# Kernel optimization log

Hardware: AMD Instinct MI355X
Metric: run time of the kernel (lower is better)

## Reference

```python
import jax, jax.numpy as jnp
import numpy as np

N, F, T, H, E = 50000, 16, 12, 64, 1600000
OUT = 1


def setup_inputs() -> dict:
    key = jax.random.key(0)
    ks = jax.random.split(key, 14)
    inp = {}
    inp["x"] = jax.random.normal(ks[0], (N, F, T), dtype=jnp.float32)
    inp["edge_index"] = jax.random.randint(ks[1], (2, E), 0, N, dtype=jnp.int32)
    inp["edge_weight"] = jax.random.uniform(ks[2], (E,), dtype=jnp.float32)
    C = F + H  # GCN input channels (x concat hidden)
    s = 0.05
    inp["Wz"] = jax.random.normal(ks[3], (C, H), dtype=jnp.float32) * s
    inp["bz"] = jnp.zeros((H,), dtype=jnp.float32)
    inp["Wr"] = jax.random.normal(ks[4], (C, H), dtype=jnp.float32) * s
    inp["br"] = jnp.zeros((H,), dtype=jnp.float32)
    inp["Wh"] = jax.random.normal(ks[5], (C, H), dtype=jnp.float32) * s
    inp["bh"] = jnp.zeros((H,), dtype=jnp.float32)
    inp["Wa"] = jax.random.normal(ks[6], (H, H), dtype=jnp.float32) * s
    inp["ba"] = jnp.zeros((H,), dtype=jnp.float32)
    inp["cv"] = jax.random.normal(ks[7], (H, 1), dtype=jnp.float32) * s
    inp["Wfc"] = jax.random.normal(ks[8], (H, OUT), dtype=jnp.float32) * s
    inp["bfc"] = jnp.zeros((OUT,), dtype=jnp.float32)
    return inp


def _gcn(xc, W, b, src, dst, ew_norm, self_norm, n):
    # PyG GCNConv: D^{-1/2}(A+I)D^{-1/2} X W + b, with self-loop weight 1
    xw = xc @ W                                   # [N, H]
    msg = xw[src] * ew_norm[:, None]              # [E, H] gather
    agg = jax.ops.segment_sum(msg, dst, num_segments=n)  # scatter-add
    return agg + self_norm[:, None] * xw + b


def reference(x, edge_index, edge_weight, Wz, bz, Wr, br, Wh, bh, Wa, ba, cv, Wfc, bfc):
    n = x.shape[0]
    src, dst = edge_index[0], edge_index[1]
    # symmetric normalization with self-loops (weight 1)
    deg = jax.ops.segment_sum(edge_weight, dst, num_segments=n) + 1.0
    dis = jax.lax.rsqrt(deg)
    ew_norm = dis[src] * edge_weight * dis[dst]
    self_norm = dis * dis

    x_seq = jnp.transpose(x, (2, 0, 1))  # [T, N, F]

    def step(h, x_t):
        xh = jnp.concatenate([x_t, h], axis=1)
        z = jax.nn.sigmoid(_gcn(xh, Wz, bz, src, dst, ew_norm, self_norm, n))
        r = jax.nn.sigmoid(_gcn(xh, Wr, br, src, dst, ew_norm, self_norm, n))
        xrh = jnp.concatenate([x_t, r * h], axis=1)
        hc = jnp.tanh(_gcn(xrh, Wh, bh, src, dst, ew_norm, self_norm, n))
        h_new = z * h + (1.0 - z) * hc
        return h_new, h_new

    h0 = jnp.zeros((n, Wz.shape[1]), dtype=x.dtype)
    _, hs_seq = jax.lax.scan(step, h0, x_seq)      # [T, N, H]

    hs_t = jnp.transpose(hs_seq, (1, 0, 2))        # [N, T, H]
    score = jnp.tanh(hs_t @ Wa + ba)               # [N, T, H]
    align = (score @ cv)[..., 0]                   # [N, T]
    alpha = jax.nn.softmax(align, axis=1)          # softmax over time
    context = jnp.einsum('nt,nth->nh', alpha, hs_t)
    out = context @ Wfc + bfc                      # [N, OUT]
    return out
```

## Files before the change

### kernel.cpp

```cpp
#include <hip/hip_runtime.h>
#include <hip/hip_fp16.h>
#include <math.h>

#define Nn 50000
#define Ff 16
#define Tt 12
#define Hh 64
#define Ee 1600000
#define Cc 80

#define SCAN_NB 98

typedef _Float16 f16x8 __attribute__((ext_vector_type(8)));
typedef float f32x4 __attribute__((ext_vector_type(4)));

static __device__ __forceinline__ float sigmoidf_(float x) { return 1.0f / (1.0f + expf(-x)); }

__global__ void k_deg(const int* __restrict__ ei, const float* __restrict__ ew,
                      unsigned long long* __restrict__ dc) {
  int e = blockIdx.x * blockDim.x + threadIdx.x;
  if (e >= Ee) return;
  int d = ei[Ee + e];
  unsigned long long pk = (1ULL << 42) + (unsigned long long)(ew[e] * 2097152.0f + 0.5f);
  atomicAdd(&dc[d], pk);
}

__global__ void k_dis(const unsigned long long* __restrict__ dc,
                      float* __restrict__ dis, int* __restrict__ cnt) {
  int i = blockIdx.x * blockDim.x + threadIdx.x;
  if (i >= Nn) return;
  unsigned long long v = dc[i];
  cnt[i] = (int)(v >> 42);
  float deg = (float)(v & ((1ULL << 42) - 1)) * (1.0f / 2097152.0f);
  dis[i] = 1.0f / sqrtf(deg + 1.0f);
}

__global__ __launch_bounds__(256) void k_scan1(const int* __restrict__ cnt,
                                               int* __restrict__ bsum) {
  __shared__ int ss[256];
  int b = blockIdx.x, t = threadIdx.x;
  int base = b * 512 + t * 2;
  int s = 0;
  if (base < Nn) s += cnt[base];
  if (base + 1 < Nn) s += cnt[base + 1];
  ss[t] = s;
  __syncthreads();
  for (int off = 128; off > 0; off >>= 1) {
    if (t < off) ss[t] += ss[t + off];
    __syncthreads();
  }
  if (t == 0) bsum[b] = ss[0];
}

__global__ __launch_bounds__(128) void k_scan2(const int* __restrict__ bsum,
                                               int* __restrict__ boff) {
  __shared__ int ss[128];
  int t = threadIdx.x;
  int v = (t < SCAN_NB) ? bsum[t] : 0;
  ss[t] = v;
  __syncthreads();
  for (int off = 1; off < 128; off <<= 1) {
    int u = (t >= off) ? ss[t - off] : 0;
    __syncthreads();
    ss[t] += u;
    __syncthreads();
  }
  if (t < SCAN_NB) boff[t] = ss[t] - v;
}

__global__ __launch_bounds__(256) void k_scan3(const int* __restrict__ cnt,
                                               const int* __restrict__ boff,
                                               int* __restrict__ rp, int* __restrict__ cur) {
  __shared__ int ss[256];
  int b = blockIdx.x, t = threadIdx.x;
  int base = b * 512 + t * 2;
  int c0 = (base < Nn) ? cnt[base] : 0;
  int c1 = (base + 1 < Nn) ? cnt[base + 1] : 0;
  int s = c0 + c1;
  ss[t] = s;
  __syncthreads();
  for (int off = 1; off < 256; off <<= 1) {
    int u = (t >= off) ? ss[t - off] : 0;
    __syncthreads();
    ss[t] += u;
    __syncthreads();
  }
  int run = boff[b] + ss[t] - s;
  if (base < Nn) { rp[base] = run; cur[base] = run; }
  if (base + 1 < Nn) { rp[base + 1] = run + c0; cur[base + 1] = run + c0; }
  if (b == 0 && t == 0) rp[Nn] = Ee;
}

__global__ void k_scatter(const int* __restrict__ ei, const float* __restrict__ ew,
                          const float* __restrict__ dis, int* __restrict__ cur,
                          int2* __restrict__ edge2) {
  int e = blockIdx.x * blockDim.x + threadIdx.x;
  if (e >= Ee) return;
  int s = ei[e];
  int d = ei[Ee + e];
  float w = ew[e] * dis[s] * dis[d];
  int pos = atomicAdd(&cur[d], 1);
  edge2[pos] = make_int2(s, __float_as_int(w));
}

__global__ void k_cvt_x(const float* __restrict__ x, __half* __restrict__ x16) {
  size_t idx = (size_t)blockIdx.x * blockDim.x + threadIdx.x;
  const size_t total = (size_t)Nn * Ff * Tt;
  if (idx < total) x16[idx] = __float2half(x[idx]);
}

__global__ void k_wfrag(const float* __restrict__ Wz, const float* __restrict__ Wr,
                        const float* __restrict__ Wh, __half* __restrict__ frag) {
  int t = blockIdx.x * 256 + threadIdx.x;
  if (t >= 12 * 3 * 64) return;
  int s = t / 192, rem = t % 192, ks = rem / 64, lane = rem % 64;
  int q = lane >> 4, nl = lane & 15;
  const float* W = (s < 4) ? Wz : (s < 8) ? Wr : Wh;
  int n0 = (s & 3) * 16;
  __half tmp[8];
#pragma unroll
  for (int j = 0; j < 8; j++) {
    int k = ks * 32 + q * 8 + j;
    float v = (k < Cc) ? W[k * Hh + n0 + nl] : 0.f;
    tmp[j] = __float2half(v);
  }
  *(uint4*)(frag + ((size_t)(s * 3 + ks) * 64 + lane) * 8) = *(uint4*)tmp;
}

__global__ void k_wfrag_a(const float* __restrict__ Wa, __half* __restrict__ fragA) {
  int t = blockIdx.x * 256 + threadIdx.x;
  if (t >= 8 * 64) return;
  int s = t >> 6, lane = t & 63;
  int tile = s >> 1, ks = s & 1;
  int q = lane >> 4, m = lane & 15;
  __half tmp[8];
#pragma unroll
  for (int j = 0; j < 8; j++) {
    int k = ks * 32 + q * 8 + j;
    tmp[j] = __float2half(Wa[k * Hh + tile * 16 + m]);
  }
  *(uint4*)(fragA + ((size_t)t) * 8) = *(uint4*)tmp;
}

__global__ __launch_bounds__(256) void k_agg_px(
    const float* __restrict__ x, const __half* __restrict__ x16, __half* __restrict__ Px16,
    const int* __restrict__ rp, const int2* __restrict__ edge2,
    const float* __restrict__ dis) {
  int i = blockIdx.x * 4 + (threadIdx.x >> 6);
  if (i >= Nn) return;
  int lane = threadIdx.x & 63;
  const int R = Ff * Tt;
  const bool act = lane < 48;
  float d = dis[i], sn = d * d;
  float a0 = 0.f, a1 = 0.f, a2 = 0.f, a3 = 0.f;
  if (act) {
    float4 sv = *(const float4*)(x + (size_t)i * R + 4 * lane);
    a0 = sn * sv.x; a1 = sn * sv.y; a2 = sn * sv.z; a3 = sn * sv.w;
  }
  int jb = rp[i], je = rp[i + 1];
  for (int j = jb; j < je; j += 2) {
    int jc1 = min(j + 1, Ee - 1);
    int2 e0 = edge2[j];
    int2 e1 = edge2[jc1];
    float w0 = __int_as_float(e0.y);
    float w1 = (j + 1 < je) ? __int_as_float(e1.y) : 0.f;
    if (act) {
      uint2 g0 = *(const uint2*)(x16 + (size_t)e0.x * R + 4 * lane);
      uint2 g1 = *(const uint2*)(x16 + (size_t)e1.x * R + 4 * lane);
      float2 p01 = __half22float2(*reinterpret_cast<const __half2*>(&g0.x));
      float2 p23 = __half22float2(*reinterpret_cast<const __half2*>(&g0.y));
      float2 q01 = __half22float2(*reinterpret_cast<const __half2*>(&g1.x));
      float2 q23 = __half22float2(*reinterpret_cast<const __half2*>(&g1.y));
      a0 = fmaf(w0, p01.x, a0); a1 = fmaf(w0, p01.y, a1);
      a2 = fmaf(w0, p23.x, a2); a3 = fmaf(w0, p23.y, a3);
      a0 = fmaf(w1, q01.x, a0); a1 = fmaf(w1, q01.y, a1);
      a2 = fmaf(w1, q23.x, a2); a3 = fmaf(w1, q23.y, a3);
    }
  }
  if (act) {
#pragma unroll
    for (int k = 0; k < 4; k++) {
      int cch = 4 * lane + k;
      int f = cch / Tt, tt = cch % Tt;
      float val = (k == 0) ? a0 : (k == 1) ? a1 : (k == 2) ? a2 : a3;
      Px16[(size_t)tt * Nn * Ff + (size_t)i * Ff + f] = __float2half(val);
    }
  }
}

__global__ __launch_bounds__(256) void k_agg64v(
    const __half* __restrict__ v, __half* __restrict__ outv,
    const int* __restrict__ rp, const int2* __restrict__ edge2,
    const float* __restrict__ dis) {
  int i = blockIdx.x * 4 + (threadIdx.x >> 6);
  if (i >= Nn) return;
  int lane = threadIdx.x & 63;
  int g = lane >> 4;
  int c = lane & 15;
  float d = dis[i], sn = d * d;
  float a0, a1, a2, a3;
  {
    const uint2 gv = *(const uint2*)(v + (size_t)i * Hh + 4 * c);
    float2 f01 = __half22float2(*reinterpret_cast<const __half2*>(&gv.x));
    float2 f23 = __half22float2(*reinterpret_cast<const __half2*>(&gv.y));
    float ws = (g == 0) ? sn : 0.f;
    a0 = ws * f01.x; a1 = ws * f01.y; a2 = ws * f23.x; a3 = ws * f23.y;
  }
  int jb = rp[i], je = rp[i + 1];
  for (int j0 = jb; j0 < je; j0 += 16) {
    int j1 = j0 + g;
    int j2 = j0 + 4 + g;
    int j3 = j0 + 8 + g;
    int j4 = j0 + 12 + g;
    int2 e1 = edge2[min(j1, Ee - 1)];
    int2 e2 = edge2[min(j2, Ee - 1)];
    int2 e3 = edge2[min(j3, Ee - 1)];
    int2 e4 = edge2[min(j4, Ee - 1)];
    float w1 = (j1 < je) ? __int_as_float(e1.y) : 0.f;
    float w2 = (j2 < je) ? __int_as_float(e2.y) : 0.f;
    float w3 = (j3 < je) ? __int_as_float(e3.y) : 0.f;
    float w4 = (j4 < je) ? __int_as_float(e4.y) : 0.f;
    const uint2 g1 = *(const uint2*)(v + (size_t)e1.x * Hh + 4 * c);
    const uint2 g2 = *(const uint2*)(v + (size_t)e2.x * Hh + 4 * c);
    const uint2 g3 = *(const uint2*)(v + (size_t)e3.x * Hh + 4 * c);
    const uint2 g4 = *(const uint2*)(v + (size_t)e4.x * Hh + 4 * c);
    float2 p01 = __half22float2(*reinterpret_cast<const __half2*>(&g1.x));
    float2 p23 = __half22float2(*reinterpret_cast<const __half2*>(&g1.y));
    float2 q01 = __half22float2(*reinterpret_cast<const __half2*>(&g2.x));
    float2 q23 = __half22float2(*reinterpret_cast<const __half2*>(&g2.y));
    float2 r01 = __half22float2(*reinterpret_cast<const __half2*>(&g3.x));
    float2 r23 = __half22float2(*reinterpret_cast<const __half2*>(&g3.y));
    float2 s01 = __half22float2(*reinterpret_cast<const __half2*>(&g4.x));
    float2 s23 = __half22float2(*reinterpret_cast<const __half2*>(&g4.y));
    a0 = fmaf(w1, p01.x, a0); a1 = fmaf(w1, p01.y, a1);
    a2 = fmaf(w1, p23.x, a2); a3 = fmaf(w1, p23.y, a3);
    a0 = fmaf(w2, q01.x, a0); a1 = fmaf(w2, q01.y, a1);
    a2 = fmaf(w2, q23.x, a2); a3 = fmaf(w2, q23.y, a3);
    a0 = fmaf(w3, r01.x, a0); a1 = fmaf(w3, r01.y, a1);
    a2 = fmaf(w3, r23.x, a2); a3 = fmaf(w3, r23.y, a3);
    a0 = fmaf(w4, s01.x, a0); a1 = fmaf(w4, s01.y, a1);
    a2 = fmaf(w4, s23.x, a2); a3 = fmaf(w4, s23.y, a3);
  }
  a0 += __shfl_xor(a0, 16, 64); a1 += __shfl_xor(a1, 16, 64);
  a2 += __shfl_xor(a2, 16, 64); a3 += __shfl_xor(a3, 16, 64);
  a0 += __shfl_xor(a0, 32, 64); a1 += __shfl_xor(a1, 32, 64);
  a2 += __shfl_xor(a2, 32, 64); a3 += __shfl_xor(a3, 32, 64);
  if (lane < 16) {
    __half2 h01, h23;
    h01.x = __float2half_rn(a0); h01.y = __float2half_rn(a1);
    h23.x = __float2half_rn(a2); h23.y = __float2half_rn(a3);
    uint2 st;
    st.x = *reinterpret_cast<unsigned int*>(&h01);
    st.y = *reinterpret_cast<unsigned int*>(&h23);
    *(uint2*)(outv + (size_t)i * Hh + 4 * c) = st;
  }
}

static __device__ __forceinline__ void stage_x16(
    __half* sX16, const __half* __restrict__ Px16t, const __half* __restrict__ P64,
    int i0, int tid) {
  if (tid < 160) {
    int n = tid / 10, r = tid % 10;
    int i = i0 + n;
    uint4 raw = (r < 2) ? *(const uint4*)(Px16t + (size_t)i * Ff + r * 8)
                        : *(const uint4*)(P64 + (size_t)i * Hh + (r - 2) * 8);
    *(uint4*)(sX16 + n * 104 + r * 8) = raw;
  } else if (tid < 208) {
    int p = tid - 160, n = p / 3, part = p % 3;
    *(uint4*)(sX16 + n * 104 + 80 + part * 8) = make_uint4(0u, 0u, 0u, 0u);
  }
}

__global__ __launch_bounds__(256) void k_gemm_zr(
    const __half* __restrict__ Px16, const __half* __restrict__ Ph16,
    const __half* __restrict__ h16, const __half* __restrict__ frag,
    const float* __restrict__ bz, const float* __restrict__ br,
    __half* __restrict__ zb16, __half* __restrict__ rh16, int tstep) {
  __shared__ __align__(16) __half sX16[16 * 104];
  const int tid = threadIdx.x;
  const int i0 = blockIdx.x * 16;
  const int wv = tid >> 6, lane = tid & 63;
  f16x8 bzf[3], brf[3];
#pragma unroll
  for (int ks = 0; ks < 3; ks++) {
    bzf[ks] = *(const f16x8*)(frag + ((size_t)(wv * 3 + ks) * 64 + lane) * 8);
    brf[ks] = *(const f16x8*)(frag + ((size_t)((4 + wv) * 3 + ks) * 64 + lane) * 8);
  }
  stage_x16(sX16, Px16 + (size_t)tstep * Nn * Ff, Ph16, i0, tid);
  __syncthreads();
  const int m = lane & 15, q = lane >> 4;
  f32x4 accz = {0.f, 0.f, 0.f, 0.f}, accr = {0.f, 0.f, 0.f, 0.f};
#pragma unroll
  for (int ks = 0; ks < 3; ks++) {
    f16x8 a = *(const f16x8*)(sX16 + m * 104 + ks * 32 + q * 8);
    accz = __builtin_amdgcn_mfma_f32_16x16x32_f16(a, bzf[ks], accz, 0, 0, 0);
    accr = __builtin_amdgcn_mfma_f32_16x16x32_f16(a, brf[ks], accr, 0, 0, 0);
  }
  const int o = wv * 16 + m;
  float bzo = bz[o], bro = br[o];
  const int nb = i0 + q * 4;
#pragma unroll
  for (int r = 0; r < 4; r++) {
    int node = nb + r;
    float zv = sigmoidf_(accz[r] + bzo);
    float rv = sigmoidf_(accr[r] + bro);
    float hv = __half2float(h16[(size_t)node * Hh + o]);
    zb16[(size_t)node * Hh + o] = __float2half(zv);
    rh16[(size_t)node * Hh + o] = __float2half(rv * hv);
  }
}

__global__ __launch_bounds__(256) void k_gemm_h(
    const __half* __restrict__ Px16, const __half* __restrict__ Prh16,
    const __half* __restrict__ zb16, float* __restrict__ h, __half* __restrict__ h16,
    __half* __restrict__ hs16, const __half* __restrict__ frag,
    const float* __restrict__ bh, int tstep) {
  __shared__ __align__(16) __half sX16[16 * 104];
  const int tid = threadIdx.x;
  const int i0 = blockIdx.x * 16;
  const int wv = tid >> 6, lane = tid & 63;
  f16x8 bf[3];
#pragma unroll
  for (int ks = 0; ks < 3; ks++)
    bf[ks] = *(const f16x8*)(frag + ((size_t)((8 + wv) * 3 + ks) * 64 + lane) * 8);
  stage_x16(sX16, Px16 + (size_t)tstep * Nn * Ff, Prh16, i0, tid);
  __syncthreads();
  const int m = lane & 15, q = lane >> 4;
  f32x4 acc = {0.f, 0.f, 0.f, 0.f};
#pragma unroll
  for (int ks = 0; ks < 3; ks++) {
    f16x8 a = *(const f16x8*)(sX16 + m * 104 + ks * 32 + q * 8);
    acc = __builtin_amdgcn_mfma_f32_16x16x32_f16(a, bf[ks], acc, 0, 0, 0);
  }
  const int o = wv * 16 + m;
  float bho = bh[o];
  const int nb = i0 + q * 4;
  __half* hst = hs16 + (size_t)tstep * Nn * Hh;
#pragma unroll
  for (int r = 0; r < 4; r++) {
    int node = nb + r;
    float hc = tanhf(acc[r] + bho);
    float zv = __half2float(zb16[(size_t)node * Hh + o]);
    float hv = h[(size_t)node * Hh + o];
    float hn = zv * hv + (1.0f - zv) * hc;
    h[(size_t)node * Hh + o] = hn;
    __half hh = __float2half(hn);
    h16[(size_t)node * Hh + o] = hh;
    hst[(size_t)node * Hh + o] = hh;
  }
}

__global__ __launch_bounds__(256) void k_att(
    const __half* __restrict__ hs16, const __half* __restrict__ fragA,
    const float* __restrict__ ba, const float* __restrict__ cv,
    const float* __restrict__ Wfc, const float* __restrict__ bfc,
    float* __restrict__ out) {
  const int tid = threadIdx.x;
  const int wv = tid >> 6, lane = tid & 63;
  const int i = blockIdx.x * 4 + wv;
  if (i >= Nn) return;
  const int m = lane & 15, q = lane >> 4;

  f16x8 bf[4][2];
#pragma unroll
  for (int s = 0; s < 8; s++)
    bf[s >> 1][s & 1] = *(const f16x8*)(fragA + (size_t)(s * 64 + lane) * 8);

  const int tm = (m < Tt) ? m : (Tt - 1);
  const __half* hbase = hs16 + (size_t)tm * Nn * Hh + (size_t)i * Hh;
  f16x8 a0 = *(const f16x8*)(hbase + q * 8);
  f16x8 a1 = *(const f16x8*)(hbase + 32 + q * 8);

  f32x4 acc[4];
#pragma unroll
  for (int tile = 0; tile < 4; tile++) acc[tile] = f32x4{0.f, 0.f, 0.f, 0.f};
#pragma unroll
  for (int tile = 0; tile < 4; tile++) {
    acc[tile] = __builtin_amdgcn_mfma_f32_16x16x32_f16(a0, bf[tile][0], acc[tile], 0, 0, 0);
    acc[tile] = __builtin_amdgcn_mfma_f32_16x16x32_f16(a1, bf[tile][1], acc[tile], 0, 0, 0);
  }

  float ba_l[4], cv_l[4];
#pragma unroll
  for (int tile = 0; tile < 4; tile++) {
    ba_l[tile] = ba[tile * 16 + m];
    cv_l[tile] = cv[tile * 16 + m];
  }
  float ar[4];
#pragma unroll
  for (int r = 0; r < 4; r++) {
    float s = 0.f;
#pragma unroll
    for (int tile = 0; tile < 4; tile++)
      s += tanhf(acc[tile][r] + ba_l[tile]) * cv_l[tile];
    s += __shfl_xor(s, 1, 64);
    s += __shfl_xor(s, 2, 64);
    s += __shfl_xor(s, 4, 64);
    s += __shfl_xor(s, 8, 64);
    ar[r] = s;
  }
  float al[Tt];
#pragma unroll
  for (int t = 0; t < Tt; t++) al[t] = __shfl(ar[t & 3], (t >> 2) * 16, 64);
  float mx = al[0];
#pragma unroll
  for (int t = 1; t < Tt; t++) mx = fmaxf(mx, al[t]);
  float ssum = 0.f;
#pragma unroll
  for (int t = 0; t < Tt; t++) { al[t] = expf(al[t] - mx); ssum += al[t]; }
  float inv = 1.0f / ssum;
  float cx = 0.f;
#pragma unroll
  for (int t = 0; t < Tt; t++)
    cx = fmaf(al[t], __half2float(hs16[(size_t)t * Nn * Hh + (size_t)i * Hh + lane]), cx);
  float p = cx * inv * Wfc[lane];
#pragma unroll
  for (int off = 32; off >= 1; off >>= 1) p += __shfl_xor(p, off, 64);
  if (lane == 0) out[i] = p + bfc[0];
}

extern "C" void kernel_launch(void* const* d_in, const int* in_sizes, int n_in,
                              void* d_out, int out_size, void* d_ws, size_t ws_size,
                              hipStream_t stream) {
  const float* x   = (const float*)d_in[0];
  const int* ei    = (const int*)d_in[1];
  const float* ew  = (const float*)d_in[2];
  const float* Wz  = (const float*)d_in[3];
  const float* bz  = (const float*)d_in[4];
  const float* Wr  = (const float*)d_in[5];
  const float* br  = (const float*)d_in[6];
  const float* Wh  = (const float*)d_in[7];
  const float* bh  = (const float*)d_in[8];
  const float* Wa  = (const float*)d_in[9];
  const float* ba  = (const float*)d_in[10];
  const float* cv  = (const float*)d_in[11];
  const float* Wfc = (const float*)d_in[12];
  const float* bfc = (const float*)d_in[13];
  float* out = (float*)d_out;

  char* w = (char*)d_ws;
  auto alloc = [&](size_t bytes) {
    char* p = w;
    w += (bytes + 255) & ~(size_t)255;
    return p;
  };
  unsigned long long* dc = (unsigned long long*)alloc((size_t)Nn * 8);
  float* dis = (float*)alloc((size_t)Nn * 4);
  int* cnt   = (int*)alloc((size_t)Nn * 4);
  int* rp    = (int*)alloc((size_t)(Nn + 1) * 4);
  int* cur   = (int*)alloc((size_t)Nn * 4);
  int* bsum  = (int*)alloc((size_t)SCAN_NB * 4);
  int* boff  = (int*)alloc((size_t)SCAN_NB * 4);
  int2* edge2 = (int2*)alloc((size_t)Ee * 8);
  __half* x16  = (__half*)alloc((size_t)Nn * Ff * Tt * 2);
  __half* Px16 = (__half*)alloc((size_t)Tt * Nn * Ff * 2);
  float* h     = (float*)alloc((size_t)Nn * Hh * 4);
  __half* h16  = (__half*)alloc((size_t)Nn * Hh * 2);
  __half* rh16 = (__half*)alloc((size_t)Nn * Hh * 2);
  __half* zb16 = (__half*)alloc((size_t)Nn * Hh * 2);
  __half* Ph16 = (__half*)alloc((size_t)Nn * Hh * 2);
  __half* Prh16 = (__half*)alloc((size_t)Nn * Hh * 2);
  __half* hs16 = (__half*)alloc((size_t)Tt * Nn * Hh * 2);
  __half* wfrag = (__half*)alloc((size_t)12 * 3 * 64 * 8 * 2);
  __half* wfragA = (__half*)alloc((size_t)8 * 64 * 8 * 2);

  hipMemsetAsync(dc, 0, (size_t)Nn * 8, stream);
  hipMemsetAsync(h, 0, (size_t)Nn * Hh * 4, stream);
  hipMemsetAsync(h16, 0, (size_t)Nn * Hh * 2, stream);

  k_deg<<<(Ee + 255) / 256, 256, 0, stream>>>(ei, ew, dc);
  k_dis<<<(Nn + 255) / 256, 256, 0, stream>>>(dc, dis, cnt);
  k_scan1<<<SCAN_NB, 256, 0, stream>>>(cnt, bsum);
  k_scan2<<<1, 128, 0, stream>>>(bsum, boff);
  k_scan3<<<SCAN_NB, 256, 0, stream>>>(cnt, boff, rp, cur);
  k_scatter<<<(Ee + 255) / 256, 256, 0, stream>>>(ei, ew, dis, cur, edge2);
  {
    const size_t total = (size_t)Nn * Ff * Tt;
    k_cvt_x<<<(int)((total + 255) / 256), 256, 0, stream>>>(x, x16);
  }
  k_wfrag<<<9, 256, 0, stream>>>(Wz, Wr, Wh, wfrag);
  k_wfrag_a<<<2, 256, 0, stream>>>(Wa, wfragA);
  k_agg_px<<<(Nn + 3) / 4, 256, 0, stream>>>(x, x16, Px16, rp, edge2, dis);

  const int gGemm = Nn / 16;
  const int gNode = (Nn + 3) / 4;
  for (int t = 0; t < Tt; t++) {
    k_agg64v<<<gNode, 256, 0, stream>>>(h16, Ph16, rp, edge2, dis);
    k_gemm_zr<<<gGemm, 256, 0, stream>>>(Px16, Ph16, h16, wfrag, bz, br, zb16, rh16, t);
    k_agg64v<<<gNode, 256, 0, stream>>>(rh16, Prh16, rp, edge2, dis);
    k_gemm_h<<<gGemm, 256, 0, stream>>>(Px16, Prh16, zb16, h, h16, hs16, wfrag, bh, t);
  }
  k_att<<<gNode, 256, 0, stream>>>(hs16, wfragA, ba, cv, Wfc, bfc, out);
}
```

Baseline: 1.540 ms.

## Fuse neighbor aggregation into GRU gate GEMM kernels via LDS staging

The separate sparse aggregation kernel is folded into the z/r and candidate GEMM kernels. Each wave now aggregates four nodes' neighbor features directly into the shared-memory tile, and that tile feeds the MFMA. This removes the aggregated intermediate buffers, their global write and read-back, and two kernel launches per timestep. The trade-off is coarser parallelism for the gather: each block does sixteen nodes, four per wave serially, so load imbalance and latency hiding may get worse.

```diff
diff --git a/kernel.cpp b/kernel.cpp
--- a/kernel.cpp
+++ b/kernel.cpp
@@ -188,13 +188,22 @@
   }
 }
 
-__global__ __launch_bounds__(256) void k_agg64v(
-    const __half* __restrict__ v, __half* __restrict__ outv,
-    const int* __restrict__ rp, const int2* __restrict__ edge2,
-    const float* __restrict__ dis) {
-  int i = blockIdx.x * 4 + (threadIdx.x >> 6);
-  if (i >= Nn) return;
-  int lane = threadIdx.x & 63;
+static __device__ __forceinline__ void stage_px_zero(
+    __half* sX16, const __half* __restrict__ Px16t, int i0, int tid) {
+  if (tid < 32) {
+    int n = tid >> 1, r = tid & 1;
+    *(uint4*)(sX16 + n * 104 + r * 8) =
+        *(const uint4*)(Px16t + (size_t)(i0 + n) * Ff + r * 8);
+  } else if (tid < 80) {
+    int p = tid - 32, n = p / 3, part = p % 3;
+    *(uint4*)(sX16 + n * 104 + 80 + part * 8) = make_uint4(0u, 0u, 0u, 0u);
+  }
+}
+
+static __device__ __forceinline__ void agg_node_to_lds(
+    __half* sX16, int n, int i, int lane,
+    const __half* __restrict__ v, const int* __restrict__ rp,
+    const int2* __restrict__ edge2, const float* __restrict__ dis) {
   int g = lane >> 4;
   int c = lane & 15;
   float d = dis[i], sn = d * d;
@@ -252,29 +261,16 @@
     uint2 st;
     st.x = *reinterpret_cast<unsigned int*>(&h01);
     st.y = *reinterpret_cast<unsigned int*>(&h23);
-    *(uint2*)(outv + (size_t)i * Hh + 4 * c) = st;
-  }
-}
-
-static __device__ __forceinline__ void stage_x16(
-    __half* sX16, const __half* __restrict__ Px16t, const __half* __restrict__ P64,
-    int i0, int tid) {
-  if (tid < 160) {
-    int n = tid / 10, r = tid % 10;
-    int i = i0 + n;
-    uint4 raw = (r < 2) ? *(const uint4*)(Px16t + (size_t)i * Ff + r * 8)
-                        : *(const uint4*)(P64 + (size_t)i * Hh + (r - 2) * 8);
-    *(uint4*)(sX16 + n * 104 + r * 8) = raw;
-  } else if (tid < 208) {
-    int p = tid - 160, n = p / 3, part = p % 3;
-    *(uint4*)(sX16 + n * 104 + 80 + part * 8) = make_uint4(0u, 0u, 0u, 0u);
-  }
-}
-
-__global__ __launch_bounds__(256) void k_gemm_zr(
-    const __half* __restrict__ Px16, const __half* __restrict__ Ph16,
-    const __half* __restrict__ h16, const __half* __restrict__ frag,
+    *(uint2*)(sX16 + n * 104 + 16 + 4 * c) = st;
+  }
+}
+
+__global__ __launch_bounds__(256) void k_zr_f(
+    const __half* __restrict__ Px16, const __half* __restrict__ h16,
+    const __half* __restrict__ frag,
     const float* __restrict__ bz, const float* __restrict__ br,
+    const int* __restrict__ rp, const int2* __restrict__ edge2,
+    const float* __restrict__ dis,
     __half* __restrict__ zb16, __half* __restrict__ rh16, int tstep) {
   __shared__ __align__(16) __half sX16[16 * 104];
   const int tid = threadIdx.x;
@@ -286,7 +282,12 @@
     bzf[ks] = *(const f16x8*)(frag + ((size_t)(wv * 3 + ks) * 64 + lane) * 8);
     brf[ks] = *(const f16x8*)(frag + ((size_t)((4 + wv) * 3 + ks) * 64 + lane) * 8);
   }
-  stage_x16(sX16, Px16 + (size_t)tstep * Nn * Ff, Ph16, i0, tid);
+  stage_px_zero(sX16, Px16 + (size_t)tstep * Nn * Ff, i0, tid);
+#pragma unroll
+  for (int k = 0; k < 4; k++) {
+    int n = wv * 4 + k;
+    agg_node_to_lds(sX16, n, i0 + n, lane, h16, rp, edge2, dis);
+  }
   __syncthreads();
   const int m = lane & 15, q = lane >> 4;
   f32x4 accz = {0.f, 0.f, 0.f, 0.f}, accr = {0.f, 0.f, 0.f, 0.f};
@@ -310,11 +311,13 @@
   }
 }
 
-__global__ __launch_bounds__(256) void k_gemm_h(
-    const __half* __restrict__ Px16, const __half* __restrict__ Prh16,
+__global__ __launch_bounds__(256) void k_h_f(
+    const __half* __restrict__ Px16, const __half* __restrict__ rh16,
     const __half* __restrict__ zb16, float* __restrict__ h, __half* __restrict__ h16,
     __half* __restrict__ hs16, const __half* __restrict__ frag,
-    const float* __restrict__ bh, int tstep) {
+    const float* __restrict__ bh,
+    const int* __restrict__ rp, const int2* __restrict__ edge2,
+    const float* __restrict__ dis, int tstep) {
   __shared__ __align__(16) __half sX16[16 * 104];
   const int tid = threadIdx.x;
   const int i0 = blockIdx.x * 16;
@@ -323,7 +326,12 @@
 #pragma unroll
   for (int ks = 0; ks < 3; ks++)
     bf[ks] = *(const f16x8*)(frag + ((size_t)((8 + wv) * 3 + ks) * 64 + lane) * 8);
-  stage_x16(sX16, Px16 + (size_t)tstep * Nn * Ff, Prh16, i0, tid);
+  stage_px_zero(sX16, Px16 + (size_t)tstep * Nn * Ff, i0, tid);
+#pragma unroll
+  for (int k = 0; k < 4; k++) {
+    int n = wv * 4 + k;
+    agg_node_to_lds(sX16, n, i0 + n, lane, rh16, rp, edge2, dis);
+  }
   __syncthreads();
   const int m = lane & 15, q = lane >> 4;
   f32x4 acc = {0.f, 0.f, 0.f, 0.f};
@@ -458,8 +466,6 @@
   __half* h16  = (__half*)alloc((size_t)Nn * Hh * 2);
   __half* rh16 = (__half*)alloc((size_t)Nn * Hh * 2);
   __half* zb16 = (__half*)alloc((size_t)Nn * Hh * 2);
-  __half* Ph16 = (__half*)alloc((size_t)Nn * Hh * 2);
-  __half* Prh16 = (__half*)alloc((size_t)Nn * Hh * 2);
   __half* hs16 = (__half*)alloc((size_t)Tt * Nn * Hh * 2);
   __half* wfrag = (__half*)alloc((size_t)12 * 3 * 64 * 8 * 2);
   __half* wfragA = (__half*)alloc((size_t)8 * 64 * 8 * 2);
@@ -485,10 +491,10 @@
   const int gGemm = Nn / 16;
   const int gNode = (Nn + 3) / 4;
   for (int t = 0; t < Tt; t++) {
-    k_agg64v<<<gNode, 256, 0, stream>>>(h16, Ph16, rp, edge2, dis);
-    k_gemm_zr<<<gGemm, 256, 0, stream>>>(Px16, Ph16, h16, wfrag, bz, br, zb16, rh16, t);
-    k_agg64v<<<gNode, 256, 0, stream>>>(rh16, Prh16, rp, edge2, dis);
-    k_gemm_h<<<gGemm, 256, 0, stream>>>(Px16, Prh16, zb16, h, h16, hs16, wfrag, bh, t);
+    k_zr_f<<<gGemm, 256, 0, stream>>>(Px16, h16, wfrag, bz, br, rp, edge2, dis,
+                                      zb16, rh16, t);
+    k_h_f<<<gGemm, 256, 0, stream>>>(Px16, rh16, zb16, h, h16, hs16, wfrag, bh,
+                                     rp, edge2, dis, t);
   }
   k_att<<<gNode, 256, 0, stream>>>(hs16, wfragA, ba, cv, Wfc, bfc, out);
 }
```

After: 1.517 ms. About the same (-1.5%).
